# Performance work log

Hardware: AMD Instinct MI355X
Metric: run time of the kernel (lower is better)

## Reference

```python
import jax, jax.numpy as jnp
import numpy as np

NEG = -1e6  # masked_softmax fill value from the original code


def setup_inputs() -> dict:
    key = jax.random.key(0)
    ks = jax.random.split(key, 8)
    B, Q, K, Dq, Dk, Dv, H = 8, 256, 1024, 256, 256, 128, 128
    queries = jax.random.normal(ks[0], (B, Q, Dq), dtype=jnp.float32)
    keys = jax.random.normal(ks[1], (B, K, Dk), dtype=jnp.float32)
    values = jax.random.normal(ks[2], (B, K, Dv), dtype=jnp.float32)
    valid_lens = jax.random.randint(ks[3], (B,), 1, K + 1, dtype=jnp.int32)
    # learned params (Dense, use_bias=False): y = x @ W
    W_q = jax.random.normal(ks[4], (Dq, H), dtype=jnp.float32) / np.sqrt(Dq)
    W_k = jax.random.normal(ks[5], (Dk, H), dtype=jnp.float32) / np.sqrt(Dk)
    w_v = jax.random.normal(ks[6], (H,), dtype=jnp.float32) / np.sqrt(H)
    return {"queries": queries, "keys": keys, "values": values,
            "valid_lens": valid_lens, "W_q": W_q, "W_k": W_k, "w_v": w_v}


def reference(queries, keys, values, valid_lens, W_q, W_k, w_v):
    q = jnp.einsum('bqd,dh->bqh', queries, W_q)          # [B,Q,H]
    k = jnp.einsum('bkd,dh->bkh', keys, W_k)             # [B,K,H]
    features = jnp.tanh(q[:, :, None, :] + k[:, None, :, :])  # [B,Q,K,H]
    scores = jnp.einsum('bqkh,h->bqk', features, w_v)    # [B,Q,K]
    # masked softmax over last axis: positions >= valid_len set to -1e6
    K_len = scores.shape[-1]
    mask = jnp.arange(K_len)[None, None, :] < valid_lens[:, None, None]
    scores = jnp.where(mask, scores, NEG)
    attn = jax.nn.softmax(scores, axis=-1)
    return jnp.einsum('bqk,bkv->bqv', attn, values)      # [B,Q,Dv]
```

## Files before the change

kernel.cpp:

```cpp
#include <hip/hip_runtime.h>
#include <hip/hip_bf16.h>

#if defined(__has_builtin)
#if __has_builtin(__builtin_amdgcn_exp2f)
#define EXP2F __builtin_amdgcn_exp2f
#endif
#if __has_builtin(__builtin_amdgcn_rcpf)
#define RCPF __builtin_amdgcn_rcpf
#endif
#endif
#ifndef EXP2F
#define EXP2F exp2f
#endif
#ifndef RCPF
#define RCPF(x) (1.0f / (x))
#endif

#define B_  8
#define Q_  256
#define K_  1024
#define D_  256
#define H_  128
#define DV_ 128

#define CSL 2.8853900817779268f
#define L2E 1.4426950408889634f

#define QE_OFF   0
#define KE_OFF   262144
#define WPK_OFF  1310720

__global__ __launch_bounds__(256) void proj_kernel(
    const float* __restrict__ queries, const float* __restrict__ keys,
    const float* __restrict__ Wq, const float* __restrict__ Wk,
    const float* __restrict__ w_v,
    float* __restrict__ qE, float2* __restrict__ kET2, float* __restrict__ wpk)
{
    __shared__ __align__(16) float As[64][68];
    __shared__ __align__(16) float Ws[64][64];

    const int tid = threadIdx.x;
    const int blk = blockIdx.x;
    const bool isQ = blk < 64;
    const int t = isQ ? blk : (blk - 64);
    const int rowtile = t >> 1;
    const int cbase = (t & 1) * 64;
    const int row0 = rowtile * 64;
    const float* A = isQ ? (queries + row0 * D_) : (keys + row0 * D_);
    const float* W = isQ ? Wq : Wk;

    float acc[4][4];
#pragma unroll
    for (int i = 0; i < 4; i++)
#pragma unroll
        for (int j = 0; j < 4; j++) acc[i][j] = 0.f;

    const int lr  = tid & 63;
    const int ldb = (tid >> 6) * 16;
    const int r4  = (tid >> 4) * 4;
    const int c4  = (tid & 15) * 4;

    for (int d0 = 0; d0 < D_; d0 += 64) {
#pragma unroll
        for (int j = 0; j < 4; j++) {
            const float4 a = *(const float4*)&A[lr * D_ + d0 + ldb + j * 4];
            As[ldb + j * 4 + 0][lr] = a.x;
            As[ldb + j * 4 + 1][lr] = a.y;
            As[ldb + j * 4 + 2][lr] = a.z;
            As[ldb + j * 4 + 3][lr] = a.w;
        }
#pragma unroll
        for (int l = 0; l < 4; l++) {
            const int idx = tid + l * 256;
            const int rr = idx >> 4, cc = (idx & 15) * 4;
            *(float4*)&Ws[rr][cc] = *(const float4*)&W[(d0 + rr) * H_ + cbase + cc];
        }
        __syncthreads();
#pragma unroll 4
        for (int d = 0; d < 64; d++) {
            const float4 a4 = *(const float4*)&As[d][r4];
            const float4 w4 = *(const float4*)&Ws[d][c4];
            const float ar[4] = {a4.x, a4.y, a4.z, a4.w};
#pragma unroll
            for (int i = 0; i < 4; i++) {
                acc[i][0] = fmaf(ar[i], w4.x, acc[i][0]);
                acc[i][1] = fmaf(ar[i], w4.y, acc[i][1]);
                acc[i][2] = fmaf(ar[i], w4.z, acc[i][2]);
                acc[i][3] = fmaf(ar[i], w4.w, acc[i][3]);
            }
        }
        __syncthreads();
    }

#pragma unroll
    for (int i = 0; i < 4; i++) {
        float e[4];
#pragma unroll
        for (int j = 0; j < 4; j++) e[j] = EXP2F(CSL * acc[i][j]);
        const int row = row0 + r4 + i;
        if (isQ) {
            *(float4*)&qE[row * H_ + cbase + c4] = make_float4(e[0], e[1], e[2], e[3]);
        } else {
            const int b = row >> 10, k = row & 1023;
            const int p0 = (cbase + c4) >> 1;
            kET2[(size_t)(b * 64 + p0) * K_ + k]     = make_float2(e[0], e[1]);
            kET2[(size_t)(b * 64 + p0 + 1) * K_ + k] = make_float2(e[2], e[3]);
        }
    }

    if (blk == 0 && tid < 64) {
        const float w1 = -2.0f * L2E * w_v[2 * tid];
        const float w2 = -2.0f * L2E * w_v[2 * tid + 1];
        *(float4*)&wpk[tid * 4] = make_float4(w1, w2, w1 + w2, 0.f);
    }
}

__global__ __launch_bounds__(512, 8) void attn_kernel(
    const float* __restrict__ qE,
    const float2* __restrict__ kET2,
    const float* __restrict__ values,
    const int*   __restrict__ valid_lens,
    const float* __restrict__ wpk,
    float* __restrict__ out)
{
    __shared__ __align__(16) float sc[K_][2];
    __shared__ __align__(16) float red[16][2][128];
    __shared__ __align__(16) float psum[8][2];
    __shared__ float rl[2];

    const int tid = threadIdx.x;
    const int b  = blockIdx.x & 7;
    const int q0 = (blockIdx.x >> 3) * 2;
    const int vl = valid_lens[b];

    const float* q0p = qE + (b * Q_ + q0) * H_;
    const float* q1p = q0p + H_;
    const int k0 = tid * 2;

    float ac00 = 0.f, ac01 = 0.f, ac10 = 0.f, ac11 = 0.f;

    if (k0 < vl) {
        const float4* kp = (const float4*)kET2 + (size_t)(b * 64) * 512 + tid;
#pragma unroll 4
        for (int p = 0; p < 64; p++) {
            const float4 v  = kp[(size_t)p * 512];
            const float4 wp = *(const float4*)&wpk[p * 4];
            const float2 qa = *(const float2*)&q0p[2 * p];
            const float2 qb = *(const float2*)&q1p[2 * p];
            {
                const float x10 = qa.x * v.x, x20 = qa.y * v.y;
                const float x11 = qa.x * v.z, x21 = qa.y * v.w;
                const float e0 = x10 + 1.f, e1 = x11 + 1.f;
                const float d0 = fmaf(e0, x20, e0), d1 = fmaf(e1, x21, e1);
                float n0 = fmaf(wp.y, x10, wp.z); n0 = fmaf(wp.x, x20, n0);
                float n1 = fmaf(wp.y, x11, wp.z); n1 = fmaf(wp.x, x21, n1);
                ac00 = fmaf(n0, RCPF(d0), ac00);
                ac01 = fmaf(n1, RCPF(d1), ac01);
            }
            {
                const float x10 = qb.x * v.x, x20 = qb.y * v.y;
                const float x11 = qb.x * v.z, x21 = qb.y * v.w;
                const float e0 = x10 + 1.f, e1 = x11 + 1.f;
                const float d0 = fmaf(e0, x20, e0), d1 = fmaf(e1, x21, e1);
                float n0 = fmaf(wp.y, x10, wp.z); n0 = fmaf(wp.x, x20, n0);
                float n1 = fmaf(wp.y, x11, wp.z); n1 = fmaf(wp.x, x21, n1);
                ac10 = fmaf(n0, RCPF(d0), ac10);
                ac11 = fmaf(n1, RCPF(d1), ac11);
            }
        }
    }

    const bool v0 = k0 < vl, v1 = (k0 + 1) < vl;
    const float p00 = v0 ? EXP2F(ac00) : 0.f;
    const float p10 = v0 ? EXP2F(ac10) : 0.f;
    const float p01 = v1 ? EXP2F(ac01) : 0.f;
    const float p11 = v1 ? EXP2F(ac11) : 0.f;
    *(float4*)&sc[k0][0] = make_float4(p00, p10, p01, p11);

    float s0 = p00 + p01, s1 = p10 + p11;
#pragma unroll
    for (int sh = 32; sh > 0; sh >>= 1) {
        s0 += __shfl_xor(s0, sh);
        s1 += __shfl_xor(s1, sh);
    }
    const int lane = tid & 63, w = tid >> 6;
    if (lane == 0) { psum[w][0] = s0; psum[w][1] = s1; }
    __syncthreads();
    if (tid < 2) {
        float tsum = 0.f;
#pragma unroll
        for (int ww = 0; ww < 8; ww++) tsum += psum[ww][tid];
        rl[tid] = RCPF(tsum);
    }

    const int vg = (tid & 31) * 4;
    const int kc = tid >> 5;
    const float* vb = values + (size_t)b * (K_ * DV_) + vg;
    float av[2][4];
#pragma unroll
    for (int q = 0; q < 2; q++)
#pragma unroll
        for (int j = 0; j < 4; j++) av[q][j] = 0.f;

    const int rem = vl - kc * 64;
    const int imax = rem <= 0 ? 0 : (rem > 64 ? 64 : rem);
#pragma unroll 2
    for (int i = 0; i < imax; i++) {
        const int k = kc * 64 + i;
        const float4 vv = *(const float4*)&vb[k * DV_];
        const float2 pp = *(const float2*)&sc[k][0];
        av[0][0] = fmaf(pp.x, vv.x, av[0][0]); av[0][1] = fmaf(pp.x, vv.y, av[0][1]);
        av[0][2] = fmaf(pp.x, vv.z, av[0][2]); av[0][3] = fmaf(pp.x, vv.w, av[0][3]);
        av[1][0] = fmaf(pp.y, vv.x, av[1][0]); av[1][1] = fmaf(pp.y, vv.y, av[1][1]);
        av[1][2] = fmaf(pp.y, vv.z, av[1][2]); av[1][3] = fmaf(pp.y, vv.w, av[1][3]);
    }
#pragma unroll
    for (int q = 0; q < 2; q++)
        *(float4*)&red[kc][q][vg] = make_float4(av[q][0], av[q][1], av[q][2], av[q][3]);
    __syncthreads();

    if (tid < 256) {
        const int q = tid >> 7, v = tid & 127;
        float tsum = 0.f;
#pragma unroll
        for (int g = 0; g < 16; g++) tsum += red[g][q][v];
        out[(b * Q_ + q0 + q) * DV_ + v] = tsum * rl[q];
    }
}

extern "C" void kernel_launch(void* const* d_in, const int* in_sizes, int n_in,
                              void* d_out, int out_size, void* d_ws, size_t ws_size,
                              hipStream_t stream) {
    const float* queries    = (const float*)d_in[0];
    const float* keys       = (const float*)d_in[1];
    const float* values     = (const float*)d_in[2];
    const int*   valid_lens = (const int*)d_in[3];
    const float* W_q        = (const float*)d_in[4];
    const float* W_k        = (const float*)d_in[5];
    const float* w_v        = (const float*)d_in[6];
    float* out = (float*)d_out;

    float*  ws   = (float*)d_ws;
    float*  qE   = ws + QE_OFF;
    float2* kET2 = (float2*)(ws + KE_OFF);
    float*  wpk  = ws + WPK_OFF;

    proj_kernel<<<320, 256, 0, stream>>>(queries, keys, W_q, W_k, w_v, qE, kET2, wpk);
    attn_kernel<<<1024, 512, 0, stream>>>(qE, kET2, values, valid_lens, wpk, out);
}
```

Baseline: 127.8 us.

## Split keys across two blocks with eight queries per block and a combine pass

The attention kernel now gives each block 8 queries and one half of the key range, with one key per thread. Each kET2 load is reused across 8 queries instead of 2, which cuts global traffic for the key projections and the values. Partial softmax sums and AV products are written to workspace, and a new combine kernel adds the two halves and normalises them. This adds a third launch and extra workspace traffic, leaves 512 blocks, and lowers the occupancy hint from 8 to 4.

```diff
diff --git a/kernel.cpp b/kernel.cpp
--- a/kernel.cpp
+++ b/kernel.cpp
@@ -29,6 +29,8 @@
 #define QE_OFF   0
 #define KE_OFF   262144
 #define WPK_OFF  1310720
+#define AVP_OFF  1310976
+#define SP_OFF   1835264
 
 __global__ __launch_bounds__(256) void proj_kernel(
     const float* __restrict__ queries, const float* __restrict__ keys,
@@ -115,117 +117,132 @@
     }
 }
 
-__global__ __launch_bounds__(512, 8) void attn_kernel(
+__global__ __launch_bounds__(512, 4) void attn_kernel(
     const float* __restrict__ qE,
     const float2* __restrict__ kET2,
     const float* __restrict__ values,
     const int*   __restrict__ valid_lens,
     const float* __restrict__ wpk,
-    float* __restrict__ out)
+    float* __restrict__ avpart,
+    float* __restrict__ spart)
 {
-    __shared__ __align__(16) float sc[K_][2];
-    __shared__ __align__(16) float red[16][2][128];
-    __shared__ __align__(16) float psum[8][2];
-    __shared__ float rl[2];
+    __shared__ __align__(16) float sc[512][8];
+    __shared__ __align__(16) float red[4][8][128];
+    __shared__ __align__(16) float psum[8][8];
 
     const int tid = threadIdx.x;
-    const int b  = blockIdx.x & 7;
-    const int q0 = (blockIdx.x >> 3) * 2;
-    const int vl = valid_lens[b];
-
-    const float* q0p = qE + (b * Q_ + q0) * H_;
-    const float* q1p = q0p + H_;
-    const int k0 = tid * 2;
-
-    float ac00 = 0.f, ac01 = 0.f, ac10 = 0.f, ac11 = 0.f;
-
-    if (k0 < vl) {
-        const float4* kp = (const float4*)kET2 + (size_t)(b * 64) * 512 + tid;
-#pragma unroll 4
+    const int raw = blockIdx.x;
+    const int kh  = raw >> 8;
+    const int j   = raw & 255;
+    const int b   = (j + kh) & 7;
+    const int qt  = j >> 3;
+    const int q0  = qt * 8;
+    const int vl  = valid_lens[b];
+    const int k   = kh * 512 + tid;
+
+    const float* qp = qE + (b * Q_ + q0) * H_;
+
+    float acc[8];
+#pragma unroll
+    for (int q = 0; q < 8; q++) acc[q] = 0.f;
+
+    if (k < vl) {
+        const float2* kb = kET2 + (size_t)(b * 64) * K_ + k;
+#pragma unroll 2
         for (int p = 0; p < 64; p++) {
-            const float4 v  = kp[(size_t)p * 512];
+            const float2 ek = kb[(size_t)p * K_];
             const float4 wp = *(const float4*)&wpk[p * 4];
-            const float2 qa = *(const float2*)&q0p[2 * p];
-            const float2 qb = *(const float2*)&q1p[2 * p];
-            {
-                const float x10 = qa.x * v.x, x20 = qa.y * v.y;
-                const float x11 = qa.x * v.z, x21 = qa.y * v.w;
-                const float e0 = x10 + 1.f, e1 = x11 + 1.f;
-                const float d0 = fmaf(e0, x20, e0), d1 = fmaf(e1, x21, e1);
-                float n0 = fmaf(wp.y, x10, wp.z); n0 = fmaf(wp.x, x20, n0);
-                float n1 = fmaf(wp.y, x11, wp.z); n1 = fmaf(wp.x, x21, n1);
-                ac00 = fmaf(n0, RCPF(d0), ac00);
-                ac01 = fmaf(n1, RCPF(d1), ac01);
+#pragma unroll
+            for (int q = 0; q < 8; q++) {
+                const float2 qq = *(const float2*)&qp[q * H_ + 2 * p];
+                const float x1 = qq.x * ek.x, x2 = qq.y * ek.y;
+                const float e1 = x1 + 1.f;
+                const float d  = fmaf(e1, x2, e1);
+                float n = fmaf(wp.y, x1, wp.z);
+                n = fmaf(wp.x, x2, n);
+                acc[q] = fmaf(n, RCPF(d), acc[q]);
             }
-            {
-                const float x10 = qb.x * v.x, x20 = qb.y * v.y;
-                const float x11 = qb.x * v.z, x21 = qb.y * v.w;
-                const float e0 = x10 + 1.f, e1 = x11 + 1.f;
-                const float d0 = fmaf(e0, x20, e0), d1 = fmaf(e1, x21, e1);
-                float n0 = fmaf(wp.y, x10, wp.z); n0 = fmaf(wp.x, x20, n0);
-                float n1 = fmaf(wp.y, x11, wp.z); n1 = fmaf(wp.x, x21, n1);
-                ac10 = fmaf(n0, RCPF(d0), ac10);
-                ac11 = fmaf(n1, RCPF(d1), ac11);
-            }
-        }
-    }
-
-    const bool v0 = k0 < vl, v1 = (k0 + 1) < vl;
-    const float p00 = v0 ? EXP2F(ac00) : 0.f;
-    const float p10 = v0 ? EXP2F(ac10) : 0.f;
-    const float p01 = v1 ? EXP2F(ac01) : 0.f;
-    const float p11 = v1 ? EXP2F(ac11) : 0.f;
-    *(float4*)&sc[k0][0] = make_float4(p00, p10, p01, p11);
-
-    float s0 = p00 + p01, s1 = p10 + p11;
+        }
+    }
+
+    const bool valid = k < vl;
+    float p8[8];
+#pragma unroll
+    for (int q = 0; q < 8; q++) p8[q] = valid ? EXP2F(acc[q]) : 0.f;
+    *(float4*)&sc[tid][0] = make_float4(p8[0], p8[1], p8[2], p8[3]);
+    *(float4*)&sc[tid][4] = make_float4(p8[4], p8[5], p8[6], p8[7]);
+
+    float s8[8];
+#pragma unroll
+    for (int q = 0; q < 8; q++) s8[q] = p8[q];
 #pragma unroll
     for (int sh = 32; sh > 0; sh >>= 1) {
-        s0 += __shfl_xor(s0, sh);
-        s1 += __shfl_xor(s1, sh);
+#pragma unroll
+        for (int q = 0; q < 8; q++) s8[q] += __shfl_xor(s8[q], sh);
     }
     const int lane = tid & 63, w = tid >> 6;
-    if (lane == 0) { psum[w][0] = s0; psum[w][1] = s1; }
+    if (lane == 0) {
+        *(float4*)&psum[w][0] = make_float4(s8[0], s8[1], s8[2], s8[3]);
+        *(float4*)&psum[w][4] = make_float4(s8[4], s8[5], s8[6], s8[7]);
+    }
     __syncthreads();
-    if (tid < 2) {
-        float tsum = 0.f;
-#pragma unroll
-        for (int ww = 0; ww < 8; ww++) tsum += psum[ww][tid];
-        rl[tid] = RCPF(tsum);
-    }
-
-    const int vg = (tid & 31) * 4;
-    const int kc = tid >> 5;
-    const float* vb = values + (size_t)b * (K_ * DV_) + vg;
+    if (tid < 8) {
+        float t = 0.f;
+#pragma unroll
+        for (int ww = 0; ww < 8; ww++) t += psum[ww][tid];
+        spart[kh * 2048 + b * Q_ + q0 + tid] = t;
+    }
+
+    const int v4  = tid & 31;
+    const int qp2 = (tid >> 5) & 3;
+    const int ks  = tid >> 7;
+    const float* vb = values + (size_t)b * (K_ * DV_) + v4 * 4;
     float av[2][4];
 #pragma unroll
-    for (int q = 0; q < 2; q++)
-#pragma unroll
-        for (int j = 0; j < 4; j++) av[q][j] = 0.f;
-
-    const int rem = vl - kc * 64;
-    const int imax = rem <= 0 ? 0 : (rem > 64 ? 64 : rem);
+    for (int qq = 0; qq < 2; qq++)
+#pragma unroll
+        for (int jj = 0; jj < 4; jj++) av[qq][jj] = 0.f;
+
+    const int kbase = kh * 512 + ks * 128;
+    const int rem = vl - kbase;
+    const int imax = rem <= 0 ? 0 : (rem > 128 ? 128 : rem);
 #pragma unroll 2
     for (int i = 0; i < imax; i++) {
-        const int k = kc * 64 + i;
-        const float4 vv = *(const float4*)&vb[k * DV_];
-        const float2 pp = *(const float2*)&sc[k][0];
+        const int kl = ks * 128 + i;
+        const float4 vv = *(const float4*)&vb[(kbase + i) * DV_];
+        const float2 pp = *(const float2*)&sc[kl][2 * qp2];
         av[0][0] = fmaf(pp.x, vv.x, av[0][0]); av[0][1] = fmaf(pp.x, vv.y, av[0][1]);
         av[0][2] = fmaf(pp.x, vv.z, av[0][2]); av[0][3] = fmaf(pp.x, vv.w, av[0][3]);
         av[1][0] = fmaf(pp.y, vv.x, av[1][0]); av[1][1] = fmaf(pp.y, vv.y, av[1][1]);
         av[1][2] = fmaf(pp.y, vv.z, av[1][2]); av[1][3] = fmaf(pp.y, vv.w, av[1][3]);
     }
-#pragma unroll
-    for (int q = 0; q < 2; q++)
-        *(float4*)&red[kc][q][vg] = make_float4(av[q][0], av[q][1], av[q][2], av[q][3]);
+    *(float4*)&red[ks][2 * qp2][v4 * 4]     = make_float4(av[0][0], av[0][1], av[0][2], av[0][3]);
+    *(float4*)&red[ks][2 * qp2 + 1][v4 * 4] = make_float4(av[1][0], av[1][1], av[1][2], av[1][3]);
     __syncthreads();
 
     if (tid < 256) {
-        const int q = tid >> 7, v = tid & 127;
-        float tsum = 0.f;
-#pragma unroll
-        for (int g = 0; g < 16; g++) tsum += red[g][q][v];
-        out[(b * Q_ + q0 + q) * DV_ + v] = tsum * rl[q];
-    }
+        const int q = tid >> 5, vv4 = tid & 31;
+        float4 t = make_float4(0.f, 0.f, 0.f, 0.f);
+#pragma unroll
+        for (int g = 0; g < 4; g++) {
+            const float4 r = *(const float4*)&red[g][q][vv4 * 4];
+            t.x += r.x; t.y += r.y; t.z += r.z; t.w += r.w;
+        }
+        *(float4*)&avpart[(size_t)(kh * 2048 + b * Q_ + q0 + q) * DV_ + vv4 * 4] = t;
+    }
+}
+
+__global__ __launch_bounds__(256) void combine_kernel(
+    const float* __restrict__ avpart, const float* __restrict__ spart,
+    float* __restrict__ out)
+{
+    const int idx = (blockIdx.x * 256 + threadIdx.x) * 4;
+    const int row = idx >> 7;
+    const float4 a0 = *(const float4*)&avpart[idx];
+    const float4 a1 = *(const float4*)&avpart[2048 * DV_ + idx];
+    const float r = RCPF(spart[row] + spart[2048 + row]);
+    *(float4*)&out[idx] = make_float4((a0.x + a1.x) * r, (a0.y + a1.y) * r,
+                                      (a0.z + a1.z) * r, (a0.w + a1.w) * r);
 }
 
 extern "C" void kernel_launch(void* const* d_in, const int* in_sizes, int n_in,
@@ -240,11 +257,14 @@
     const float* w_v        = (const float*)d_in[6];
     float* out = (float*)d_out;
 
-    float*  ws   = (float*)d_ws;
-    float*  qE   = ws + QE_OFF;
-    float2* kET2 = (float2*)(ws + KE_OFF);
-    float*  wpk  = ws + WPK_OFF;
+    float*  ws     = (float*)d_ws;
+    float*  qE     = ws + QE_OFF;
+    float2* kET2   = (float2*)(ws + KE_OFF);
+    float*  wpk    = ws + WPK_OFF;
+    float*  avpart = ws + AVP_OFF;
+    float*  spart  = ws + SP_OFF;
 
     proj_kernel<<<320, 256, 0, stream>>>(queries, keys, W_q, W_k, w_v, qE, kET2, wpk);
-    attn_kernel<<<1024, 512, 0, stream>>>(qE, kET2, values, valid_lens, wpk, out);
-}
+    attn_kernel<<<512, 512, 0, stream>>>(qE, kET2, values, valid_lens, wpk, avpart, spart);
+    combine_kernel<<<256, 256, 0, stream>>>(avpart, spart, out);
+}
```

Result: slower. 143.5 us (+12.3%).
